# Kernel tuning notes

Hardware: AMD Instinct MI355X
Metric: run time of the kernel (lower is better)

Reference implementation:

```python
import jax, jax.numpy as jnp
import numpy as np

# static config (mirrors init_kwargs)
FS = 512          # frame_seqlen
NFPB = 2          # num_frame_per_block
NIB = 3           # num image/action/state blocks
NAPB = 32         # num_action_per_block
NSPB = 1          # num_state_per_block
LOCAL = 4         # local_attn_size (frames)
FIRST = FS
IMGB = NIB * NFPB * FS
ALEN = NIB * NAPB
SLEN = NIB * NSPB
TOTAL = FIRST + IMGB + ALEN + SLEN   # 3683
DIM = 1536
NH = 12
HD = DIM // NH    # 128
EPS = 1e-6


def _build_mask():
    # faithful port of _visualize_attention_mask (the block-sparse pattern)
    m = np.zeros((TOTAL, TOTAL), dtype=bool)
    fi0, fi1 = 0, FIRST
    ib0, ib1 = fi1, fi1 + IMGB
    a0, a1 = ib1, ib1 + ALEN
    s0 = a1
    m[fi0:fi1, fi0:fi1] = True  # first image: self only (sink)
    for b in range(NIB):
        bs = ib0 + b * NFPB * FS
        be = ib0 + (b + 1) * NFPB * FS
        m[bs:be, fi0:fi1] = True                      # sink
        kv = max(ib0, be - LOCAL * FS)                # local window
        m[bs:be, kv:be] = True
        m[bs:be, a0 + b * NAPB:a0 + (b + 1) * NAPB] = True
        m[bs:be, s0 + b * NSPB:s0 + (b + 1) * NSPB] = True
    for b in range(NIB):
        ab0 = a0 + b * NAPB
        ab1 = a0 + (b + 1) * NAPB
        m[ab0:ab1, fi0:fi1] = True
        ibe = ib0 + (b + 1) * NFPB * FS
        kv = max(ib0, ibe - LOCAL * FS)
        m[ab0:ab1, kv:ibe] = True
        m[ab0:ab1, ab0:ab1] = True
        m[ab0:ab1, s0 + b * NSPB:s0 + (b + 1) * NSPB] = True
    for b in range(NIB):
        ss = s0 + b * NSPB
        se = s0 + (b + 1) * NSPB
        m[ss:se, ss:se] = True
    return m

_MASK = jnp.asarray(_build_mask())


def _rms_norm(x, g):
    # WanRMSNorm over full dim, fp32 accumulation
    v = jnp.mean(jnp.square(x.astype(jnp.float32)), axis=-1, keepdims=True)
    return (x.astype(jnp.float32) * jax.lax.rsqrt(v + EPS)).astype(x.dtype) * g


def _rope(x, cos, sin):
    # x: [B,L,n,hd]; pairs are consecutive (..., hd//2, 2)
    B, L, n, d = x.shape
    xp = x.reshape(B, L, n, d // 2, 2)
    xr, xi = xp[..., 0], xp[..., 1]
    c = cos[None, :, None, :]
    s = sin[None, :, None, :]
    yr = xr * c - xi * s
    yi = xr * s + xi * c
    return jnp.stack([yr, yi], axis=-1).reshape(B, L, n, d)


def setup_inputs() -> dict:
    key = jax.random.key(0)
    ks = jax.random.split(key, 16)
    x = jax.random.normal(ks[0], (1, TOTAL, DIM), jnp.float32)

    def mkfreq(k, L):
        ang = jax.random.uniform(k, (L, HD // 2), jnp.float32, 0.0, 2.0 * np.pi)
        return jnp.stack([jnp.cos(ang), jnp.sin(ang)], axis=-1).reshape(L, HD)

    freqs = mkfreq(ks[1], FIRST + IMGB)
    freqs_action = mkfreq(ks[2], ALEN)
    freqs_state = mkfreq(ks[3], SLEN)
    sc = 1.0 / np.sqrt(DIM)
    Wq = jax.random.normal(ks[4], (DIM, DIM), jnp.float32) * sc
    Wk = jax.random.normal(ks[5], (DIM, DIM), jnp.float32) * sc
    Wv = jax.random.normal(ks[6], (DIM, DIM), jnp.float32) * sc
    Wo = jax.random.normal(ks[7], (DIM, DIM), jnp.float32) * sc
    bq = jax.random.normal(ks[8], (DIM,), jnp.float32) * 0.01
    bk = jax.random.normal(ks[9], (DIM,), jnp.float32) * 0.01
    bv = jax.random.normal(ks[10], (DIM,), jnp.float32) * 0.01
    bo = jax.random.normal(ks[11], (DIM,), jnp.float32) * 0.01
    gq = jnp.ones((DIM,), jnp.float32)
    gk = jnp.ones((DIM,), jnp.float32)
    return {"x": x, "freqs": freqs, "freqs_action": freqs_action,
            "freqs_state": freqs_state, "Wq": Wq, "bq": bq, "Wk": Wk, "bk": bk,
            "Wv": Wv, "bv": bv, "Wo": Wo, "bo": bo, "gq": gq, "gk": gk}


def reference(x, freqs, freqs_action, freqs_state, Wq, bq, Wk, bk, Wv, bv, Wo, bo, gq, gk):
    B, L, _ = x.shape
    q = _rms_norm(x @ Wq + bq, gq).reshape(B, L, NH, HD)
    k = _rms_norm(x @ Wk + bk, gk).reshape(B, L, NH, HD)
    v = (x @ Wv + bv).reshape(B, L, NH, HD)
    # full-sequence rope: image freqs then action freqs then state freqs
    f = jnp.concatenate([freqs, freqs_action, freqs_state], axis=0).reshape(L, HD // 2, 2)
    cos, sin = f[..., 0], f[..., 1]
    q = _rope(q, cos, sin)
    k = _rope(k, cos, sin)
    scores = jnp.einsum('bqnd,bknd->bnqk', q, k) / np.sqrt(HD)
    scores = jnp.where(_MASK[None, None], scores, jnp.finfo(scores.dtype).min)
    p = jax.nn.softmax(scores, axis=-1)
    o = jnp.einsum('bnqk,bknd->bqnd', p, v).reshape(B, L, DIM)
    return o @ Wo + bo
```

## Files before the change

kernel.cpp:

```cpp
#include <hip/hip_runtime.h>

#define LSEQ 3683
#define LPAD 3840
#define DIMSZ 1536
#define NHEAD 12
#define HEADD 128
#define SM_SCALE 0.088388347648318447f

typedef unsigned short u16;
typedef unsigned int u32;
typedef __bf16 bf16x8 __attribute__((ext_vector_type(8)));
typedef float f32x4 __attribute__((ext_vector_type(4)));

__device__ __forceinline__ u16 f2b(float f) {
  u32 u = __float_as_uint(f);
  u += 0x7FFFu + ((u >> 16) & 1u);
  return (u16)(u >> 16);
}
__device__ __forceinline__ float b2f(u16 s) {
  return __uint_as_float(((u32)s) << 16);
}
__device__ __forceinline__ int imax(int a, int b) { return a > b ? a : b; }

__device__ __forceinline__ void gl_lds16(const u16* g, u16* l) {
  __builtin_amdgcn_global_load_lds((const __attribute__((address_space(1))) u32*)g,
                                   (__attribute__((address_space(3))) u32*)l,
                                   16, 0, 0);
}

__device__ __forceinline__ int xcd_swz(int orig, int nwg) {
  int q = nwg >> 3, r = nwg & 7;
  int x = orig & 7, l = orig >> 3;
  return (x < r ? x * (q + 1) : r * (q + 1) + (x - r) * q) + l;
}

__global__ void convert_x_kernel(const float* __restrict__ x, u16* __restrict__ xb) {
  long idx = (long)blockIdx.x * blockDim.x + threadIdx.x;
  long base = idx * 4;
  if (base >= (long)LPAD * DIMSZ) return;
  float4 v;
  if (base < (long)LSEQ * DIMSZ) v = *(const float4*)(x + base);
  else v = make_float4(0.f, 0.f, 0.f, 0.f);
  ushort4 o;
  o.x = f2b(v.x); o.y = f2b(v.y); o.z = f2b(v.z); o.w = f2b(v.w);
  *(ushort4*)(xb + base) = o;
}

__global__ void transpose_w_kernel(const float* __restrict__ W0, const float* __restrict__ W1,
                                   const float* __restrict__ W2, const float* __restrict__ W3,
                                   u16* __restrict__ Wt) {
  const float* W = (blockIdx.z == 0) ? W0 : (blockIdx.z == 1) ? W1 : (blockIdx.z == 2) ? W2 : W3;
  u16* dst = Wt + (size_t)blockIdx.z * DIMSZ * DIMSZ;
  __shared__ float tile[32][33];
  int k0 = blockIdx.x * 32, n0 = blockIdx.y * 32;
  int tx = threadIdx.x & 31, ty = threadIdx.x >> 5;
  #pragma unroll
  for (int i = 0; i < 4; i++) {
    int k = k0 + ty + i * 8;
    tile[ty + i * 8][tx] = W[(size_t)k * DIMSZ + n0 + tx];
  }
  __syncthreads();
  #pragma unroll
  for (int i = 0; i < 4; i++) {
    int n = n0 + ty + i * 8;
    dst[(size_t)n * DIMSZ + k0 + tx] = f2b(tile[tx][ty + i * 8]);
  }
}

#define BAR() __builtin_amdgcn_s_barrier()
#define LGK0() asm volatile("s_waitcnt lgkmcnt(0)" ::: "memory")
#define LGK8() asm volatile("s_waitcnt lgkmcnt(8)" ::: "memory")
#define VMC9() asm volatile("s_waitcnt vmcnt(9)" ::: "memory")
#define VMC6() asm volatile("s_waitcnt vmcnt(6)" ::: "memory")
#define VMC0() asm volatile("s_waitcnt vmcnt(0)" ::: "memory")
#define PRIO1() __builtin_amdgcn_s_setprio(1)
#define PRIO0() __builtin_amdgcn_s_setprio(0)

#define STG_A(buf, q, kt) \
  gl_lds16(gA + (size_t)((q) * 64) * DIMSZ + (kt), &Asg[buf][((q) * 64 + w * 8) * 64]);
#define STG_B(buf, q, kt) \
  gl_lds16(gB + (size_t)((q) * 64) * DIMSZ + (kt), &Bsg[buf][((q) * 64 + w * 8) * 64]);

#define LDA3(buf, mh) { \
  _Pragma("unroll") for (int mf = 0; mf < 3; mf++) { \
    int rb = (wm * 96 + (mh) * 48 + mf * 16) * 64; \
    Ar[mf * 2 + 0] = *(const bf16x8*)&Asg[buf][rb + off0]; \
    Ar[mf * 2 + 1] = *(const bf16x8*)&Asg[buf][rb + off1]; } }
#define LDB3(buf, nh) { \
  _Pragma("unroll") for (int nf = 0; nf < 3; nf++) { \
    int rb = (wn * 96 + (nh) * 48 + nf * 16) * 64; \
    Br[nh][nf * 2 + 0] = *(const bf16x8*)&Bsg[buf][rb + off0]; \
    Br[nh][nf * 2 + 1] = *(const bf16x8*)&Bsg[buf][rb + off1]; } }

#define MFMAQ3(mh, nh) { \
  _Pragma("unroll") for (int mf = 0; mf < 3; mf++) \
    _Pragma("unroll") for (int nf = 0; nf < 3; nf++) { \
      acc[(mh)*3+mf][(nh)*3+nf] = __builtin_amdgcn_mfma_f32_16x16x32_bf16(Ar[mf*2+0], Br[nh][nf*2+0], acc[(mh)*3+mf][(nh)*3+nf], 0, 0, 0); \
      acc[(mh)*3+mf][(nh)*3+nf] = __builtin_amdgcn_mfma_f32_16x16x32_bf16(Ar[mf*2+1], Br[nh][nf*2+1], acc[(mh)*3+mf][(nh)*3+nf], 0, 0, 0); } }

__launch_bounds__(512, 2)
__global__ void gemm_qkv384_kernel(const u16* __restrict__ A, const u16* __restrict__ Wt,
                                   const float* __restrict__ bq, const float* __restrict__ bk,
                                   const float* __restrict__ bv,
                                   u16* __restrict__ Qb, u16* __restrict__ Kb,
                                   u16* __restrict__ Vt) {
  __shared__ __align__(16) u16 Asg[2][384 * 64];
  __shared__ __align__(16) u16 Bsg[2][192 * 64];

  int wg = xcd_swz(blockIdx.x, 10 * 24);
  int nt = wg % 24;
  int m0 = (wg / 24) * 384;
  int which = nt >> 3;
  const float* bias = (which == 0) ? bq : (which == 1) ? bk : bv;

  int t = threadIdx.x;
  int lane = t & 63, w = t >> 6;
  int c = lane & 15, g = lane >> 4;
  int wm = w >> 1, wn = w & 1;

  int srow = t >> 3;
  int schunk = ((t & 7) ^ (srow & 7)) * 8;
  const u16* gA = A + (size_t)(m0 + srow) * DIMSZ + schunk;
  const u16* gB = Wt + (size_t)(nt * 192 + srow) * DIMSZ + schunk;

  int off0 = c * 64 + ((g) ^ (c & 7)) * 8;
  int off1 = c * 64 + ((g + 4) ^ (c & 7)) * 8;

  f32x4 acc[6][6];
  f32x4 zero = {0.f, 0.f, 0.f, 0.f};
  #pragma unroll
  for (int am = 0; am < 6; am++)
    #pragma unroll
    for (int an = 0; an < 6; an++) acc[am][an] = zero;
  bf16x8 Ar[6];
  bf16x8 Br[2][6];

  STG_B(0, 0, 0) STG_B(0, 1, 0) STG_B(0, 2, 0)
  STG_A(0, 0, 0) STG_A(0, 1, 0) STG_A(0, 2, 0)
  STG_A(0, 3, 0) STG_A(0, 4, 0) STG_A(0, 5, 0)
  STG_B(1, 0, 64) STG_B(1, 1, 64) STG_B(1, 2, 64)
  STG_A(1, 0, 64) STG_A(1, 1, 64) STG_A(1, 2, 64)
  STG_A(1, 3, 64) STG_A(1, 4, 64) STG_A(1, 5, 64)
  VMC9();
  BAR();

  for (int i = 0; i < DIMSZ / 64 / 2 - 1; ++i) {
    int kt2 = (2 * i + 2) * 64;
    int kt3 = (2 * i + 3) * 64;
    LDA3(0, 0) LDB3(0, 0)
    LGK8(); BAR(); LGK0();
    PRIO1(); MFMAQ3(0, 0) PRIO0();
    BAR();
    LDB3(0, 1)
    BAR(); LGK0();
    PRIO1(); MFMAQ3(0, 1) PRIO0();
    BAR();
    LDA3(0, 1)
    STG_B(0, 0, kt2) STG_B(0, 1, kt2) STG_B(0, 2, kt2)
    BAR(); LGK0();
    PRIO1(); MFMAQ3(1, 1) PRIO0();
    BAR();
    STG_A(0, 0, kt2) STG_A(0, 1, kt2) STG_A(0, 2, kt2)
    VMC6(); BAR();
    PRIO1(); MFMAQ3(1, 0) PRIO0();
    BAR();
    LDA3(1, 0) LDB3(1, 0)
    STG_A(0, 3, kt2) STG_A(0, 4, kt2) STG_A(0, 5, kt2)
    LGK8(); BAR(); LGK0();
    PRIO1(); MFMAQ3(0, 0) PRIO0();
    BAR();
    LDB3(1, 1)
    BAR(); LGK0();
    PRIO1(); MFMAQ3(0, 1) PRIO0();
    BAR();
    LDA3(1, 1)
    STG_B(1, 0, kt3) STG_B(1, 1, kt3) STG_B(1, 2, kt3)
    BAR(); LGK0();
    PRIO1(); MFMAQ3(1, 1) PRIO0();
    BAR();
    STG_A(1, 0, kt3) STG_A(1, 1, kt3) STG_A(1, 2, kt3)
    STG_A(1, 3, kt3) STG_A(1, 4, kt3) STG_A(1, 5, kt3)
    VMC9(); BAR();
    PRIO1(); MFMAQ3(1, 0) PRIO0();
    BAR();
  }

  {
    LDA3(0, 0) LDB3(0, 0)
    LGK8(); BAR(); LGK0();
    PRIO1(); MFMAQ3(0, 0) PRIO0();
    BAR();
    LDB3(0, 1)
    BAR(); LGK0();
    PRIO1(); MFMAQ3(0, 1) PRIO0();
    BAR();
    LDA3(0, 1)
    BAR(); LGK0();
    PRIO1(); MFMAQ3(1, 1) PRIO0();
    BAR();
    VMC0(); BAR();
    PRIO1(); MFMAQ3(1, 0) PRIO0();
    BAR();
    LDA3(1, 0) LDB3(1, 0)
    LGK8(); BAR(); LGK0();
    PRIO1(); MFMAQ3(0, 0) PRIO0();
    BAR();
    LDB3(1, 1)
    BAR(); LGK0();
    PRIO1(); MFMAQ3(0, 1) PRIO0();
    BAR();
    LDA3(1, 1)
    BAR(); LGK0();
    PRIO1(); MFMAQ3(1, 1) PRIO0();
    MFMAQ3(1, 0)
  }

  #pragma unroll
  for (int an = 0; an < 6; an++) {
    int ncol = (nt & 7) * 192 + wn * 96 + (an / 3) * 48 + (an % 3) * 16 + c;
    float bvv = bias[ncol];
    #pragma unroll
    for (int am = 0; am < 6; am++) {
      int rowb = m0 + wm * 96 + (am / 3) * 48 + (am % 3) * 16 + 4 * g;
      if (which == 2) {
        ushort4 pv;
        pv.x = f2b(acc[am][an][0] + bvv);
        pv.y = f2b(acc[am][an][1] + bvv);
        pv.z = f2b(acc[am][an][2] + bvv);
        pv.w = f2b(acc[am][an][3] + bvv);
        *(ushort4*)&Vt[(size_t)ncol * LPAD + rowb] = pv;
      } else {
        u16* P = (which == 1) ? Kb : Qb;
        #pragma unroll
        for (int r = 0; r < 4; r++)
          P[(size_t)(rowb + r) * DIMSZ + ncol] = f2b(acc[am][an][r] + bvv);
      }
    }
  }
}

#define GEMM_PROLOGUE()                                                          \
  __shared__ __align__(16) u16 As[4][128 * 32];                                  \
  __shared__ __align__(16) u16 Bs[4][128 * 32];                                  \
  int t = threadIdx.x;                                                           \
  int lane = t & 63, w = t >> 6;                                                 \
  int g = lane >> 4, c = lane & 15;                                              \
  int wm = w >> 1, wn = w & 1;                                                   \
  f32x4 acc[4][4];                                                               \
  f32x4 zero = {0.f, 0.f, 0.f, 0.f};                                             \
  _Pragma("unroll") for (int fr = 0; fr < 4; fr++)                               \
      _Pragma("unroll") for (int fc = 0; fc < 4; fc++) acc[fr][fc] = zero;       \
  int srcc = (((lane & 3) ^ ((lane >> 2) & 3))) * 8;    \
  const u16* gA = A + (size_t)(m0 + w * 32 + (lane >> 2)) * DIMSZ + srcc;        \
  const u16* gB = Bt + (size_t)(n0 + w * 32 + (lane >> 2)) * DIMSZ + srcc;       \
  int gsw = (g ^ (c & 3)) * 8;

#define GEMM_STAGE(buf, kt)                                                      \
  _Pragma("unroll") for (int q = 0; q < 2; q++) {                                \
    gl_lds16(gA + (size_t)(q * 16) * DIMSZ + (kt), &As[buf][(w * 32 + q * 16) * 32]); \
    gl_lds16(gB + (size_t)(q * 16) * DIMSZ + (kt), &Bs[buf][(w * 32 + q * 16) * 32]); \
  }

#define GEMM_COMPUTE(buf)                                                        \
  {                                                                              \
    bf16x8 af[4], bfr[4];                                                        \
    _Pragma("unroll") for (int fr = 0; fr < 4; fr++)                             \
        af[fr] = *(const bf16x8*)&As[buf][(wm * 64 + fr * 16 + c) * 32 + gsw];   \
    _Pragma("unroll") for (int fc = 0; fc < 4; fc++)                             \
        bfr[fc] = *(const bf16x8*)&Bs[buf][(wn * 64 + fc * 16 + c) * 32 + gsw];  \
    _Pragma("unroll") for (int fr = 0; fr < 4; fr++)                             \
        _Pragma("unroll") for (int fc = 0; fc < 4; fc++)                         \
            acc[fr][fc] = __builtin_amdgcn_mfma_f32_16x16x32_bf16(af[fr], bfr[fc], acc[fr][fc], 0, 0, 0); \
  }

#define GEMM_MAINLOOP()                                                          \
  GEMM_STAGE(0, 0)                                                               \
  GEMM_STAGE(1, 32)                                                              \
  GEMM_STAGE(2, 64)                                                              \
  {                                                                              \
    const int nk = DIMSZ / 32;                                                   \
    for (int ki = 0; ki < nk; ki++) {                                            \
      int rem = nk - ki;                                                         \
      if (rem > 2)      asm volatile("s_waitcnt vmcnt(8)" ::: "memory");         \
      else if (rem == 2) asm volatile("s_waitcnt vmcnt(4)" ::: "memory");        \
      else               asm volatile("s_waitcnt vmcnt(0)" ::: "memory");        \
      __builtin_amdgcn_s_barrier();                                              \
      if (ki + 3 < nk) { GEMM_STAGE((ki + 3) & 3, (ki + 3) * 32) }               \
      GEMM_COMPUTE(ki & 3)                                                       \
    }                                                                            \
  }

__launch_bounds__(256)
__global__ void gemm_out_kernel(const u16* __restrict__ A, const u16* __restrict__ Bt,
                                const float* __restrict__ bias, float* __restrict__ outF) {
  int wg = xcd_swz(blockIdx.x, 29 * 12);
  int n0 = (wg % 12) * 128;
  int m0 = (wg / 12) * 128;

  GEMM_PROLOGUE()
  GEMM_MAINLOOP()

  #pragma unroll
  for (int fc = 0; fc < 4; fc++) {
    int col = n0 + wn * 64 + fc * 16 + c;
    float bvv = bias[col];
    #pragma unroll
    for (int fr = 0; fr < 4; fr++) {
      int rowb = m0 + wm * 64 + fr * 16 + 4 * g;
      #pragma unroll
      for (int r = 0; r < 4; r++) {
        int row = rowb + r;
        if (row < LSEQ) outF[(size_t)row * DIMSZ + col] = acc[fr][fc][r] + bvv;
      }
    }
  }
}

__launch_bounds__(256)
__global__ void normrope_kernel(u16* __restrict__ Qb, u16* __restrict__ Kb,
                                const float* __restrict__ gq, const float* __restrict__ gk,
                                const float* __restrict__ freqs, const float* __restrict__ freqs_a,
                                const float* __restrict__ freqs_s) {
  int l = blockIdx.x;
  int sel = blockIdx.y;
  u16* P = sel ? Kb : Qb;
  const float* gvec = sel ? gk : gq;
  int t = threadIdx.x;
  u16* row = P + (size_t)l * DIMSZ;
  float xv[6];
  #pragma unroll
  for (int i = 0; i < 3; i++) {
    int p = i * 256 + t;
    ushort2 u = *(const ushort2*)(row + 2 * p);
    xv[2 * i] = b2f(u.x);
    xv[2 * i + 1] = b2f(u.y);
  }
  float ss = 0.f;
  #pragma unroll
  for (int i = 0; i < 6; i++) ss += xv[i] * xv[i];
  #pragma unroll
  for (int d = 32; d; d >>= 1) ss += __shfl_down(ss, d);
  __shared__ float red[4];
  __shared__ float rshare;
  if ((t & 63) == 0) red[t >> 6] = ss;
  __syncthreads();
  if (t == 0) rshare = rsqrtf((red[0] + red[1] + red[2] + red[3]) * (1.0f / DIMSZ) + 1e-6f);
  __syncthreads();
  float rms = rshare;

  const float* f = (l < 3584) ? (freqs + (size_t)l * HEADD)
                : (l < 3680) ? (freqs_a + (size_t)(l - 3584) * HEADD)
                             : (freqs_s + (size_t)(l - 3680) * HEADD);
  #pragma unroll
  for (int i = 0; i < 3; i++) {
    int p = i * 256 + t;
    int j = p & 63;
    float2 csn = *(const float2*)(f + 2 * j);
    float2 gv = *(const float2*)(gvec + 2 * p);
    float xr = xv[2 * i] * rms * gv.x;
    float xi = xv[2 * i + 1] * rms * gv.y;
    ushort2 o;
    o.x = f2b(xr * csn.x - xi * csn.y);
    o.y = f2b(xr * csn.y + xi * csn.x);
    *(ushort2*)(row + 2 * p) = o;
  }
}

#define PSLOT_U16 16640
__launch_bounds__(256, 2)
__global__ void attn_dense_kernel(const u16* __restrict__ Q, const u16* __restrict__ K,
                                  const u16* __restrict__ Vt, u16* __restrict__ O,
                                  u16* __restrict__ DP) {
  __shared__ __align__(16) u16 Ks[2][32 * 144];
  __shared__ __align__(16) u16 Vs[2][128 * 40];
  __shared__ __align__(16) u16 Pl[4][32 * 40];

  int bx = blockIdx.x;
  int qbase, h, part, nparts, fb;
  if (bx < 48) { qbase = (bx / 12) * 128; h = bx % 12; part = 0; nparts = 1; fb = -1; }
  else if (bx < 336) { int i = bx - 48; int qb = i / 36; h = (i / 3) % 12; part = i % 3; nparts = 3; fb = 0; qbase = 512 + qb * 128; }
  else if (bx < 720) { int i = bx - 336; int qb = i / 48; h = (i / 4) % 12; part = i % 4; nparts = 4; fb = 1; qbase = 1536 + qb * 128; }
  else { int i = bx - 720; int qb = i / 48; h = (i / 4) % 12; part = i % 4; nparts = 4; fb = 2; qbase = 2560 + qb * 128; }

  int S0, E0, S1, E1, S2, E2, S3, E3, niv;
  if (fb < 0) { S0 = 0; E0 = 512; S1 = E1 = S2 = E2 = S3 = E3 = 0; niv = 1; }
  else {
    int be = 512 + (fb + 1) * 1024;
    int kv = imax(512, be - 2048);
    S0 = 0; E0 = 512; S1 = kv; E1 = be;
    S2 = 3584 + 32 * fb; E2 = S2 + 32; S3 = 3680 + fb; E3 = S3 + 1; niv = 4;
  }
  int B0 = S0 & ~31, B1 = S1 & ~31, B2 = S2 & ~31, B3 = S3 & ~31;
  int T1 = (E0 - B0 + 31) >> 5;
  int T2 = T1 + ((niv > 1) ? ((E1 - B1 + 31) >> 5) : 0);
  int T3 = T2 + ((niv > 2) ? ((E2 - B2 + 31) >> 5) : 0);
  int T4 = T3 + ((niv > 3) ? ((E3 - B3 + 31) >> 5) : 0);
  int ntile = T4;
  int rlo = (ntile * part) / nparts, rhi = (ntile * (part + 1)) / nparts;

  auto tile_of = [&](int f, int& k0, int& lo, int& hi) {
    k0 = B0 + (f << 5); lo = S0; hi = E0;
    if (niv > 1 && f >= T1) { k0 = B1 + ((f - T1) << 5); lo = S1; hi = E1; }
    if (niv > 2 && f >= T2) { k0 = B2 + ((f - T2) << 5); lo = S2; hi = E2; }
    if (niv > 3 && f >= T3) { k0 = B3 + ((f - T3) << 5); lo = S3; hi = E3; }
  };

  int T = threadIdx.x;
  int lane = T & 63, w = T >> 6, g = lane >> 4, c = lane & 15;

  const u16* kgp = K + (size_t)(T >> 3) * DIMSZ + h * HEADD + 8 * (T & 7);
  int kds = (T >> 3) * 144 + 8 * (T & 7);
  const u16* vgp = Vt + ((size_t)h * HEADD + (T >> 1)) * LPAD + 16 * (T & 1);
  int vds = (T >> 1) * 40 + 16 * (T & 1);

  uint4 sk0, sk1, sv0, sv1;
  auto stage_load = [&](int k0) {
    const u16* kp = kgp + (size_t)k0 * DIMSZ;
    sk0 = *(const uint4*)(kp);
    sk1 = *(const uint4*)(kp + 64);
    sv0 = *(const uint4*)(vgp + k0);
    sv1 = *(const uint4*)(vgp + k0 + 8);
  };
  auto stage_write = [&](int buf) {
    *(uint4*)&Ks[buf][kds] = sk0;
    *(uint4*)&Ks[buf][kds + 64] = sk1;
    *(uint4*)&Vs[buf][vds] = sv0;
    *(uint4*)&Vs[buf][vds + 8] = sv1;
  };

  int qrow0 = qbase + 32 * w;
  bf16x8 qf[2][4];
  #pragma unroll
  for (int a = 0; a < 2; a++) {
    const u16* qp = Q + (size_t)(qrow0 + a * 16 + c) * DIMSZ + h * HEADD + 8 * g;
    #pragma unroll
    for (int s = 0; s < 4; s++) qf[a][s] = *(const bf16x8*)(qp + 32 * s);
  }

  f32x4 zero = {0.f, 0.f, 0.f, 0.f};
  f32x4 acc[2][8];
  f32x4 lacc[2];
  #pragma unroll
  for (int a = 0; a < 2; a++) {
    lacc[a] = zero;
    #pragma unroll
    for (int cc = 0; cc < 8; cc++) acc[a][cc] = zero;
  }
  bf16x8 onesv;
  {
    u16 ob = 0x3F80;
    #pragma unroll
    for (int i = 0; i < 8; i++) onesv[i] = ((const __bf16*)&ob)[0];
  }

  u16* Pw = &Pl[w][0];
  const float c1 = SM_SCALE * 1.44269504088896340f;
  const float c2 = 12.0f * 1.44269504088896340f;

  {
    int k0, lo, hi; tile_of(rlo, k0, lo, hi);
    stage_load(k0);
    stage_write(0);
  }
  __syncthreads();
  int cur = 0;

  for (int t = rlo; t < rhi; ++t) {
    int ck0, clo, chi; tile_of(t, ck0, clo, chi);
    bool pre = (t + 1 < rhi);
    if (pre) { int nk0, nl, nh; tile_of(t + 1, nk0, nl, nh); stage_load(nk0); }

    f32x4 sc[2][2];
    sc[0][0] = zero; sc[0][1] = zero; sc[1][0] = zero; sc[1][1] = zero;
    #pragma unroll
    for (int k2 = 0; k2 < 2; k2++)
      #pragma unroll
      for (int s = 0; s < 4; s++) {
        bf16x8 kf = *(const bf16x8*)&Ks[cur][(16 * k2 + c) * 144 + 32 * s + 8 * g];
        sc[0][k2] = __builtin_amdgcn_mfma_f32_16x16x32_bf16(qf[0][s], kf, sc[0][k2], 0, 0, 0);
        sc[1][k2] = __builtin_amdgcn_mfma_f32_16x16x32_bf16(qf[1][s], kf, sc[1][k2], 0, 0, 0);
      }

    #pragma unroll
    for (int a = 0; a < 2; a++)
      #pragma unroll
      for (int k2 = 0; k2 < 2; k2++) {
        int k = ck0 + k2 * 16 + c;
        bool valid = (k >= clo) && (k < chi);
        #pragma unroll
        for (int r = 0; r < 4; r++) {
          float p = exp2f(sc[a][k2][r] * c1 - c2);
          Pw[(a * 16 + 4 * g + r) * 40 + k2 * 16 + c] = valid ? f2b(p) : (u16)0;
        }
      }
    asm volatile("s_waitcnt lgkmcnt(0)" ::: "memory");
    __builtin_amdgcn_sched_barrier(0);

    bf16x8 pa0 = *(const bf16x8*)&Pw[c * 40 + 8 * g];
    bf16x8 pa1 = *(const bf16x8*)&Pw[(16 + c) * 40 + 8 * g];

    #pragma unroll
    for (int cc = 0; cc < 8; cc++) {
      bf16x8 vf = *(const bf16x8*)&Vs[cur][(cc * 16 + c) * 40 + 8 * g];
      acc[0][cc] = __builtin_amdgcn_mfma_f32_16x16x32_bf16(pa0, vf, acc[0][cc], 0, 0, 0);
      acc[1][cc] = __builtin_amdgcn_mfma_f32_16x16x32_bf16(pa1, vf, acc[1][cc], 0, 0, 0);
    }
    lacc[0] = __builtin_amdgcn_mfma_f32_16x16x32_bf16(pa0, onesv, lacc[0], 0, 0, 0);
    lacc[1] = __builtin_amdgcn_mfma_f32_16x16x32_bf16(pa1, onesv, lacc[1], 0, 0, 0);

    if (pre) stage_write(cur ^ 1);
    __syncthreads();
    cur ^= 1;
  }

  if (nparts == 1) {
    float inv[2][4];
    #pragma unroll
    for (int a = 0; a < 2; a++)
      #pragma unroll
      for (int r = 0; r < 4; r++) inv[a][r] = (lacc[a][r] > 0.f) ? 1.0f / lacc[a][r] : 0.f;
    #pragma unroll
    for (int a = 0; a < 2; a++)
      #pragma unroll
      for (int cc = 0; cc < 8; cc++)
        #pragma unroll
        for (int r = 0; r < 4; r++) {
          int row = qrow0 + a * 16 + 4 * g + r;
          O[(size_t)row * DIMSZ + h * HEADD + cc * 16 + c] = f2b(acc[a][cc][r] * inv[a][r]);
        }
  } else {
    int qb = (qbase - 512 - fb * 1024) >> 7;
    int sbase = (fb == 0) ? 0 : (fb == 1 ? 288 : 672);
    int slot = sbase + (qb * 12 + h) * nparts + part;
    u16* DPs = DP + (size_t)slot * PSLOT_U16;
    float* lout = (float*)(DPs + 16384);
    #pragma unroll
    for (int a = 0; a < 2; a++) {
      #pragma unroll
      for (int cc = 0; cc < 8; cc++)
        #pragma unroll
        for (int r = 0; r < 4; r++)
          DPs[(32 * w + a * 16 + 4 * g + r) * 128 + cc * 16 + c] = f2b(acc[a][cc][r]);
      if (c == 0)
        #pragma unroll
        for (int r = 0; r < 4; r++) lout[32 * w + a * 16 + 4 * g + r] = lacc[a][r];
    }
  }
}

__launch_bounds__(256)
__global__ void attn_merge_dense(const u16* __restrict__ DP, u16* __restrict__ O) {
  int qi = blockIdx.x, h = blockIdx.y;
  int fb = qi >> 3, qb = qi & 7;
  int nparts = (fb == 0) ? 3 : 4;
  int sbase = (fb == 0) ? 0 : (fb == 1 ? 288 : 672);
  int slot0 = sbase + (qb * 12 + h) * nparts;
  int qbase = 512 + fb * 1024 + qb * 128;
  int T = threadIdx.x;
  int row = T >> 1, c0 = 64 * (T & 1);

  float sum[64];
  #pragma unroll
  for (int j = 0; j < 64; j++) sum[j] = 0.f;
  float l = 0.f;
  for (int p = 0; p < nparts; p++) {
    const u16* S = DP + (size_t)(slot0 + p) * PSLOT_U16;
    l += ((const float*)(S + 16384))[row];
    #pragma unroll
    for (int j = 0; j < 64; j += 8) {
      uint4 v = *(const uint4*)&S[row * 128 + c0 + j];
      const u16* pv = (const u16*)&v;
      #pragma unroll
      for (int q = 0; q < 8; q++) sum[j + q] += b2f(pv[q]);
    }
  }
  float inv = (l > 0.f) ? 1.0f / l : 0.f;
  u16 tmp[64];
  #pragma unroll
  for (int j = 0; j < 64; j++) tmp[j] = f2b(sum[j] * inv);
  u16* op = O + (size_t)(qbase + row) * DIMSZ + h * HEADD + c0;
  #pragma unroll
  for (int j = 0; j < 64; j += 8) *(uint4*)(op + j) = *(uint4*)&tmp[j];
}

__launch_bounds__(256, 2)
__global__ void attn_tail_kernel(const u16* __restrict__ Q, const u16* __restrict__ K,
                                 const u16* __restrict__ Vt, u16* __restrict__ O,
                                 float* __restrict__ Part) {
  __shared__ __align__(16) char smem[20608];
  __shared__ float Lsum[32];

  int bx = blockIdx.x;
  int h = blockIdx.y;
  int qt, part;
  if (bx < 3) { qt = 112 + bx; part = 0; }
  else if (bx < 6) { qt = 112 + (bx - 3); part = 1; }
  else { qt = 115; part = 0; }
  int qbase = qt * 32;
  bool heavy = (qt <= 114);

  int t = threadIdx.x, lane = t & 63, w = t >> 6, g = lane >> 4, c = lane & 15;

  int S0, E0, S1, E1, S2, E2, S3, E3, niv;
  if (qbase < 3680) {
    int b = (qbase - 3584) >> 5;
    int ibe = 512 + (b + 1) * 1024;
    int kv = imax(512, ibe - 2048);
    S0 = 0; E0 = 512; S1 = kv; E1 = ibe;
    S2 = 3584 + 32 * b; E2 = S2 + 32; S3 = 3680 + b; E3 = S3 + 1; niv = 4;
  } else {
    S0 = 3680; E0 = 3683; S1 = S2 = S3 = 0; E1 = E2 = E3 = 0; niv = 1;
  }
  bool diag = (qbase >= 3680);

  int B0 = S0 & ~31, B1 = S1 & ~31, B2 = S2 & ~31, B3 = S3 & ~31;
  int T1 = (E0 - B0 + 31) >> 5;
  int T2 = T1 + ((niv > 1) ? ((E1 - B1 + 31) >> 5) : 0);
  int T3 = T2 + ((niv > 2) ? ((E2 - B2 + 31) >> 5) : 0);
  int T4 = T3 + ((niv > 3) ? ((E3 - B3 + 31) >> 5) : 0);
  int ntile = T4;

  int rlo = 0, rhi = ntile;
  if (heavy) { int half = (ntile + 1) >> 1; if (part == 0) rhi = half; else rlo = half; }

  auto tile_of = [&](int f, int& k0, int& lo, int& hi) {
    k0 = B0 + (f << 5); lo = S0; hi = E0;
    if (niv > 1 && f >= T1) { k0 = B1 + ((f - T1) << 5); lo = S1; hi = E1; }
    if (niv > 2 && f >= T2) { k0 = B2 + ((f - T2) << 5); lo = S2; hi = E2; }
    if (niv > 3 && f >= T3) { k0 = B3 + ((f - T3) << 5); lo = S3; hi = E3; }
  };

  bf16x8 qf[2][4];
  #pragma unroll
  for (int a = 0; a < 2; a++) {
    const u16* qp = Q + (size_t)(qbase + a * 16 + c) * DIMSZ + h * HEADD + 8 * g;
    #pragma unroll
    for (int s = 0; s < 4; s++) qf[a][s] = *(const bf16x8*)(qp + 32 * s);
  }

  f32x4 zero = {0.f, 0.f, 0.f, 0.f};
  f32x4 acc[2][8];
  f32x4 lacc[2];
  #pragma unroll
  for (int a = 0; a < 2; a++) {
    lacc[a] = zero;
    #pragma unroll
    for (int cc = 0; cc < 8; cc++) acc[a][cc] = zero;
  }
  bf16x8 onesv;
  {
    u16 ob = 0x3F80;
    #pragma unroll
    for (int i = 0; i < 8; i++) onesv[i] = ((const __bf16*)&ob)[0];
  }

  u16* PwA = (u16*)smem + w * 2560;
  u16* PwB = PwA + 1280;

  bf16x8 kc[2][4], vbuf[8], pa0, pa1;
  const float c1 = SM_SCALE * 1.44269504088896340f;
  const float c2 = 12.0f * 1.44269504088896340f;

  auto loadK = [&](int k0) {
    #pragma unroll
    for (int k2 = 0; k2 < 2; k2++) {
      const u16* kp = K + (size_t)(k0 + 16 * k2 + c) * DIMSZ + h * HEADD + 8 * g;
      #pragma unroll
      for (int s = 0; s < 4; s++) kc[k2][s] = *(const bf16x8*)(kp + 32 * s);
    }
  };
  auto loadV = [&](int k0) {
    #pragma unroll
    for (int cc = 0; cc < 8; cc++)
      vbuf[cc] = *(const bf16x8*)(Vt + (size_t)(h * HEADD + cc * 16 + c) * LPAD + k0 + 8 * g);
  };
  auto QKf = [&](f32x4 (&sc)[2][2]) {
    sc[0][0] = zero; sc[0][1] = zero; sc[1][0] = zero; sc[1][1] = zero;
    #pragma unroll
    for (int k2 = 0; k2 < 2; k2++)
      #pragma unroll
      for (int s = 0; s < 4; s++) {
        sc[0][k2] = __builtin_amdgcn_mfma_f32_16x16x32_bf16(qf[0][s], kc[k2][s], sc[0][k2], 0, 0, 0);
        sc[1][k2] = __builtin_amdgcn_mfma_f32_16x16x32_bf16(qf[1][s], kc[k2][s], sc[1][k2], 0, 0, 0);
      }
  };
  auto smstore = [&](f32x4 (&sc)[2][2], int k0, int lo, int hi, u16* Pw) {
    #pragma unroll
    for (int a = 0; a < 2; a++)
      #pragma unroll
      for (int k2 = 0; k2 < 2; k2++) {
        int k = k0 + k2 * 16 + c;
        bool valid = (k >= lo) && (k < hi);
        #pragma unroll
        for (int r = 0; r < 4; r++) {
          float p = exp2f(sc[a][k2][r] * c1 - c2);
          bool v = valid;
          if (diag) { int qr = qbase + a * 16 + 4 * g + r; v = v && (k == qr); }
          Pw[(a * 16 + 4 * g + r) * 40 + k2 * 16 + c] = v ? f2b(p) : (u16)0;
        }
      }
  };
  auto readP = [&](u16* Pw) {
    pa0 = *(const bf16x8*)&Pw[c * 40 + 8 * g];
    pa1 = *(const bf16x8*)&Pw[(16 + c) * 40 + 8 * g];
  };
  auto PV = [&]() {
    #pragma unroll
    for (int cc = 0; cc < 8; cc++) {
      acc[0][cc] = __builtin_amdgcn_mfma_f32_16x16x32_bf16(pa0, vbuf[cc], acc[0][cc], 0, 0, 0);
      acc[1][cc] = __builtin_amdgcn_mfma_f32_16x16x32_bf16(pa1, vbuf[cc], acc[1][cc], 0, 0, 0);
    }
    lacc[0] = __builtin_amdgcn_mfma_f32_16x16x32_bf16(pa0, onesv, lacc[0], 0, 0, 0);
    lacc[1] = __builtin_amdgcn_mfma_f32_16x16x32_bf16(pa1, onesv, lacc[1], 0, 0, 0);
  };

  int i = rlo + w;
  if (i < rhi) {
    int ik0, ilo, ihi; tile_of(i, ik0, ilo, ihi);
    loadK(ik0);
    loadV(ik0);
    {
      f32x4 sc[2][2]; QKf(sc);
      smstore(sc, ik0, ilo, ihi, PwA);
    }
    asm volatile("s_waitcnt lgkmcnt(0)" ::: "memory");
    __builtin_amdgcn_sched_barrier(0);
    readP(PwA);
    int nx = i + 4;
    int nk0 = 0, nlo = 0, nhi = 0;
    bool useB = true;
    if (nx < rhi) { tile_of(nx, nk0, nlo, nhi); loadK(nk0); }
    while (nx < rhi) {
      int ck0 = nk0, clo = nlo, chi = nhi;
      f32x4 sc[2][2]; QKf(sc);
      int nn = nx + 4;
      if (nn < rhi) { tile_of(nn, nk0, nlo, nhi); loadK(nk0); }
      u16* Pw = useB ? PwB : PwA;
      smstore(sc, ck0, clo, chi, Pw);
      PV();
      loadV(ck0);
      asm volatile("s_waitcnt lgkmcnt(0)" ::: "memory");
      __builtin_amdgcn_sched_barrier(0);
      readP(Pw);
      useB = !useB;
      i = nx; nx = nn;
    }
    PV();
  }

  __syncthreads();
  float* Oacc = (float*)smem;
  if (w == 0) {
    #pragma unroll
    for (int a = 0; a < 2; a++) {
      #pragma unroll
      for (int cc = 0; cc < 8; cc++)
        #pragma unroll
        for (int r = 0; r < 4; r++)
          Oacc[(a * 16 + 4 * g + r) * 132 + cc * 16 + c] = acc[a][cc][r];
      if (c == 0)
        #pragma unroll
        for (int r = 0; r < 4; r++) Lsum[a * 16 + 4 * g + r] = lacc[a][r];
    }
  }
  __syncthreads();
  #pragma unroll
  for (int ww = 1; ww < 4; ww++) {
    if (w == ww) {
      #pragma unroll
      for (int a = 0; a < 2; a++) {
        #pragma unroll
        for (int cc = 0; cc < 8; cc++)
          #pragma unroll
          for (int r = 0; r < 4; r++)
            Oacc[(a * 16 + 4 * g + r) * 132 + cc * 16 + c] += acc[a][cc][r];
        if (c == 0)
          #pragma unroll
          for (int r = 0; r < 4; r++) Lsum[a * 16 + 4 * g + r] += lacc[a][r];
      }
    }
    __syncthreads();
  }

  int row = t >> 3, c0 = (t & 7) * 16;
  if (heavy) {
    size_t slot = ((size_t)((qt - 112) * 12 + h)) * 2 + part;
    float* P = Part + slot * 4160;
    #pragma unroll
    for (int j = 0; j < 16; j += 4)
      *(float4*)&P[row * 128 + c0 + j] = *(float4*)&Oacc[row * 132 + c0 + j];
    if ((t & 7) == 0) P[4096 + row] = Lsum[row];
  } else {
    int orow = qbase + row;
    if (orow < LSEQ) {
      float lsv = Lsum[row];
      float inv = (lsv > 0.f) ? 1.0f / lsv : 0.f;
      u16 tmp[16];
      #pragma unroll
      for (int j = 0; j < 16; j++) tmp[j] = f2b(Oacc[row * 132 + c0 + j] * inv);
      u16* op = O + (size_t)orow * DIMSZ + h * HEADD + c0;
      *(uint4*)(op) = *(uint4*)&tmp[0];
      *(uint4*)(op + 8) = *(uint4*)&tmp[8];
    }
  }
}

__launch_bounds__(256)
__global__ void attn_merge_tail(const float* __restrict__ Part, u16* __restrict__ O) {
  int b = blockIdx.x, h = blockIdx.y;
  const float* A = Part + ((size_t)(b * 12 + h)) * 2 * 4160;
  const float* B = A + 4160;
  int t = threadIdx.x;
  int row = t >> 3, c0 = (t & 7) * 16;
  float l = A[4096 + row] + B[4096 + row];
  float inv = (l > 0.f) ? 1.0f / l : 0.f;
  int orow = 3584 + b * 32 + row;
  u16 tmp[16];
  #pragma unroll
  for (int jj = 0; jj < 16; jj += 4) {
    float4 va = *(const float4*)&A[row * 128 + c0 + jj];
    float4 vb = *(const float4*)&B[row * 128 + c0 + jj];
    tmp[jj + 0] = f2b((va.x + vb.x) * inv);
    tmp[jj + 1] = f2b((va.y + vb.y) * inv);
    tmp[jj + 2] = f2b((va.z + vb.z) * inv);
    tmp[jj + 3] = f2b((va.w + vb.w) * inv);
  }
  u16* op = O + (size_t)orow * DIMSZ + h * HEADD + c0;
  *(uint4*)(op) = *(uint4*)&tmp[0];
  *(uint4*)(op + 8) = *(uint4*)&tmp[8];
}

extern "C" void kernel_launch(void* const* d_in, const int* in_sizes, int n_in,
                              void* d_out, int out_size, void* d_ws, size_t ws_size,
                              hipStream_t stream) {
  (void)in_sizes; (void)n_in; (void)out_size; (void)ws_size;
  const float* x       = (const float*)d_in[0];
  const float* freqs   = (const float*)d_in[1];
  const float* freqs_a = (const float*)d_in[2];
  const float* freqs_s = (const float*)d_in[3];
  const float* Wq = (const float*)d_in[4];
  const float* bq = (const float*)d_in[5];
  const float* Wk = (const float*)d_in[6];
  const float* bk = (const float*)d_in[7];
  const float* Wv = (const float*)d_in[8];
  const float* bv = (const float*)d_in[9];
  const float* Wo = (const float*)d_in[10];
  const float* bo = (const float*)d_in[11];
  const float* gq = (const float*)d_in[12];
  const float* gk = (const float*)d_in[13];
  float* out = (float*)d_out;

  char* ws = (char*)d_ws;
  size_t off = 0;
  auto alloc = [&](size_t bytes) -> void* {
    void* p = ws + off;
    off += (bytes + 255) & ~(size_t)255;
    return p;
  };
  u16* xb   = (u16*)alloc((size_t)LPAD * DIMSZ * 2);
  u16* Wt   = (u16*)alloc((size_t)4 * DIMSZ * DIMSZ * 2);
  u16* Qb   = (u16*)alloc((size_t)LPAD * DIMSZ * 2);
  u16* Kb   = (u16*)alloc((size_t)LPAD * DIMSZ * 2);
  u16* Vt   = (u16*)alloc((size_t)DIMSZ * LPAD * 2);
  u16* Ob   = (u16*)alloc((size_t)LPAD * DIMSZ * 2);
  u16* DP   = (u16*)alloc((size_t)1056 * PSLOT_U16 * 2);
  float* PartT = (float*)alloc((size_t)3 * 12 * 2 * 4160 * 4);

  convert_x_kernel<<<(LPAD * DIMSZ / 4 + 255) / 256, 256, 0, stream>>>(x, xb);
  transpose_w_kernel<<<dim3(48, 48, 4), 256, 0, stream>>>(Wq, Wk, Wv, Wo, Wt);

  gemm_qkv384_kernel<<<dim3(240), 512, 0, stream>>>(xb, Wt, bq, bk, bv, Qb, Kb, Vt);

  normrope_kernel<<<dim3(LSEQ, 2), 256, 0, stream>>>(Qb, Kb, gq, gk, freqs, freqs_a, freqs_s);

  attn_dense_kernel<<<dim3(1104), 256, 0, stream>>>(Qb, Kb, Vt, Ob, DP);
  attn_tail_kernel<<<dim3(7, 12), 256, 0, stream>>>(Qb, Kb, Vt, Ob, PartT);
  attn_merge_dense<<<dim3(24, 12), 256, 0, stream>>>(DP, Ob);
  attn_merge_tail<<<dim3(3, 12), 256, 0, stream>>>(PartT, Ob);

  gemm_out_kernel<<<dim3(29 * 12), 256, 0, stream>>>(Ob, Wt + 3 * (size_t)DIMSZ * DIMSZ, bo, out);
}
```

Before: 256.6 us.

## Reuse 384x192 pipelined GEMM for output projection and streamline softmax exp

The QKV GEMM body is factored into a macro and reused for the output projection, which now runs 80 large 384x192 tiles with 512 threads instead of 348 128x128 tiles. The attention kernels switch to the hardware exp2 intrinsic, add a fast path that skips per-element masking when a key chunk is fully valid, and shrink the K shared-memory row pitch from 144 to 136. The output GEMM trades block count for per-block reuse, so the GPU may be underfilled with only 80 workgroups. The changed K pitch alters the LDS bank-conflict pattern, and the exp2 intrinsic gives slightly different precision.

```diff
diff --git a/kernel.cpp b/kernel.cpp
--- a/kernel.cpp
+++ b/kernel.cpp
@@ -98,6 +98,85 @@
       acc[(mh)*3+mf][(nh)*3+nf] = __builtin_amdgcn_mfma_f32_16x16x32_bf16(Ar[mf*2+0], Br[nh][nf*2+0], acc[(mh)*3+mf][(nh)*3+nf], 0, 0, 0); \
       acc[(mh)*3+mf][(nh)*3+nf] = __builtin_amdgcn_mfma_f32_16x16x32_bf16(Ar[mf*2+1], Br[nh][nf*2+1], acc[(mh)*3+mf][(nh)*3+nf], 0, 0, 0); } }
 
+#define GEMM384_BODY() \
+  STG_B(0, 0, 0) STG_B(0, 1, 0) STG_B(0, 2, 0) \
+  STG_A(0, 0, 0) STG_A(0, 1, 0) STG_A(0, 2, 0) \
+  STG_A(0, 3, 0) STG_A(0, 4, 0) STG_A(0, 5, 0) \
+  STG_B(1, 0, 64) STG_B(1, 1, 64) STG_B(1, 2, 64) \
+  STG_A(1, 0, 64) STG_A(1, 1, 64) STG_A(1, 2, 64) \
+  STG_A(1, 3, 64) STG_A(1, 4, 64) STG_A(1, 5, 64) \
+  VMC9(); \
+  BAR(); \
+  for (int i = 0; i < DIMSZ / 64 / 2 - 1; ++i) { \
+    int kt2 = (2 * i + 2) * 64; \
+    int kt3 = (2 * i + 3) * 64; \
+    LDA3(0, 0) LDB3(0, 0) \
+    LGK8(); BAR(); LGK0(); \
+    PRIO1(); MFMAQ3(0, 0) PRIO0(); \
+    BAR(); \
+    LDB3(0, 1) \
+    BAR(); LGK0(); \
+    PRIO1(); MFMAQ3(0, 1) PRIO0(); \
+    BAR(); \
+    LDA3(0, 1) \
+    STG_B(0, 0, kt2) STG_B(0, 1, kt2) STG_B(0, 2, kt2) \
+    BAR(); LGK0(); \
+    PRIO1(); MFMAQ3(1, 1) PRIO0(); \
+    BAR(); \
+    STG_A(0, 0, kt2) STG_A(0, 1, kt2) STG_A(0, 2, kt2) \
+    VMC6(); BAR(); \
+    PRIO1(); MFMAQ3(1, 0) PRIO0(); \
+    BAR(); \
+    LDA3(1, 0) LDB3(1, 0) \
+    STG_A(0, 3, kt2) STG_A(0, 4, kt2) STG_A(0, 5, kt2) \
+    LGK8(); BAR(); LGK0(); \
+    PRIO1(); MFMAQ3(0, 0) PRIO0(); \
+    BAR(); \
+    LDB3(1, 1) \
+    BAR(); LGK0(); \
+    PRIO1(); MFMAQ3(0, 1) PRIO0(); \
+    BAR(); \
+    LDA3(1, 1) \
+    STG_B(1, 0, kt3) STG_B(1, 1, kt3) STG_B(1, 2, kt3) \
+    BAR(); LGK0(); \
+    PRIO1(); MFMAQ3(1, 1) PRIO0(); \
+    BAR(); \
+    STG_A(1, 0, kt3) STG_A(1, 1, kt3) STG_A(1, 2, kt3) \
+    STG_A(1, 3, kt3) STG_A(1, 4, kt3) STG_A(1, 5, kt3) \
+    VMC9(); BAR(); \
+    PRIO1(); MFMAQ3(1, 0) PRIO0(); \
+    BAR(); \
+  } \
+  { \
+    LDA3(0, 0) LDB3(0, 0) \
+    LGK8(); BAR(); LGK0(); \
+    PRIO1(); MFMAQ3(0, 0) PRIO0(); \
+    BAR(); \
+    LDB3(0, 1) \
+    BAR(); LGK0(); \
+    PRIO1(); MFMAQ3(0, 1) PRIO0(); \
+    BAR(); \
+    LDA3(0, 1) \
+    BAR(); LGK0(); \
+    PRIO1(); MFMAQ3(1, 1) PRIO0(); \
+    BAR(); \
+    VMC0(); BAR(); \
+    PRIO1(); MFMAQ3(1, 0) PRIO0(); \
+    BAR(); \
+    LDA3(1, 0) LDB3(1, 0) \
+    LGK8(); BAR(); LGK0(); \
+    PRIO1(); MFMAQ3(0, 0) PRIO0(); \
+    BAR(); \
+    LDB3(1, 1) \
+    BAR(); LGK0(); \
+    PRIO1(); MFMAQ3(0, 1) PRIO0(); \
+    BAR(); \
+    LDA3(1, 1) \
+    BAR(); LGK0(); \
+    PRIO1(); MFMAQ3(1, 1) PRIO0(); \
+    MFMAQ3(1, 0) \
+  }
+
 __launch_bounds__(512, 2)
 __global__ void gemm_qkv384_kernel(const u16* __restrict__ A, const u16* __restrict__ Wt,
                                    const float* __restrict__ bq, const float* __restrict__ bk,
@@ -135,85 +214,7 @@
   bf16x8 Ar[6];
   bf16x8 Br[2][6];
 
-  STG_B(0, 0, 0) STG_B(0, 1, 0) STG_B(0, 2, 0)
-  STG_A(0, 0, 0) STG_A(0, 1, 0) STG_A(0, 2, 0)
-  STG_A(0, 3, 0) STG_A(0, 4, 0) STG_A(0, 5, 0)
-  STG_B(1, 0, 64) STG_B(1, 1, 64) STG_B(1, 2, 64)
-  STG_A(1, 0, 64) STG_A(1, 1, 64) STG_A(1, 2, 64)
-  STG_A(1, 3, 64) STG_A(1, 4, 64) STG_A(1, 5, 64)
-  VMC9();
-  BAR();
-
-  for (int i = 0; i < DIMSZ / 64 / 2 - 1; ++i) {
-    int kt2 = (2 * i + 2) * 64;
-    int kt3 = (2 * i + 3) * 64;
-    LDA3(0, 0) LDB3(0, 0)
-    LGK8(); BAR(); LGK0();
-    PRIO1(); MFMAQ3(0, 0) PRIO0();
-    BAR();
-    LDB3(0, 1)
-    BAR(); LGK0();
-    PRIO1(); MFMAQ3(0, 1) PRIO0();
-    BAR();
-    LDA3(0, 1)
-    STG_B(0, 0, kt2) STG_B(0, 1, kt2) STG_B(0, 2, kt2)
-    BAR(); LGK0();
-    PRIO1(); MFMAQ3(1, 1) PRIO0();
-    BAR();
-    STG_A(0, 0, kt2) STG_A(0, 1, kt2) STG_A(0, 2, kt2)
-    VMC6(); BAR();
-    PRIO1(); MFMAQ3(1, 0) PRIO0();
-    BAR();
-    LDA3(1, 0) LDB3(1, 0)
-    STG_A(0, 3, kt2) STG_A(0, 4, kt2) STG_A(0, 5, kt2)
-    LGK8(); BAR(); LGK0();
-    PRIO1(); MFMAQ3(0, 0) PRIO0();
-    BAR();
-    LDB3(1, 1)
-    BAR(); LGK0();
-    PRIO1(); MFMAQ3(0, 1) PRIO0();
-    BAR();
-    LDA3(1, 1)
-    STG_B(1, 0, kt3) STG_B(1, 1, kt3) STG_B(1, 2, kt3)
-    BAR(); LGK0();
-    PRIO1(); MFMAQ3(1, 1) PRIO0();
-    BAR();
-    STG_A(1, 0, kt3) STG_A(1, 1, kt3) STG_A(1, 2, kt3)
-    STG_A(1, 3, kt3) STG_A(1, 4, kt3) STG_A(1, 5, kt3)
-    VMC9(); BAR();
-    PRIO1(); MFMAQ3(1, 0) PRIO0();
-    BAR();
-  }
-
-  {
-    LDA3(0, 0) LDB3(0, 0)
-    LGK8(); BAR(); LGK0();
-    PRIO1(); MFMAQ3(0, 0) PRIO0();
-    BAR();
-    LDB3(0, 1)
-    BAR(); LGK0();
-    PRIO1(); MFMAQ3(0, 1) PRIO0();
-    BAR();
-    LDA3(0, 1)
-    BAR(); LGK0();
-    PRIO1(); MFMAQ3(1, 1) PRIO0();
-    BAR();
-    VMC0(); BAR();
-    PRIO1(); MFMAQ3(1, 0) PRIO0();
-    BAR();
-    LDA3(1, 0) LDB3(1, 0)
-    LGK8(); BAR(); LGK0();
-    PRIO1(); MFMAQ3(0, 0) PRIO0();
-    BAR();
-    LDB3(1, 1)
-    BAR(); LGK0();
-    PRIO1(); MFMAQ3(0, 1) PRIO0();
-    BAR();
-    LDA3(1, 1)
-    BAR(); LGK0();
-    PRIO1(); MFMAQ3(1, 1) PRIO0();
-    MFMAQ3(1, 0)
-  }
+  GEMM384_BODY()
 
   #pragma unroll
   for (int an = 0; an < 6; an++) {
@@ -239,78 +240,51 @@
   }
 }
 
-#define GEMM_PROLOGUE()                                                          \
-  __shared__ __align__(16) u16 As[4][128 * 32];                                  \
-  __shared__ __align__(16) u16 Bs[4][128 * 32];                                  \
-  int t = threadIdx.x;                                                           \
-  int lane = t & 63, w = t >> 6;                                                 \
-  int g = lane >> 4, c = lane & 15;                                              \
-  int wm = w >> 1, wn = w & 1;                                                   \
-  f32x4 acc[4][4];                                                               \
-  f32x4 zero = {0.f, 0.f, 0.f, 0.f};                                             \
-  _Pragma("unroll") for (int fr = 0; fr < 4; fr++)                               \
-      _Pragma("unroll") for (int fc = 0; fc < 4; fc++) acc[fr][fc] = zero;       \
-  int srcc = (((lane & 3) ^ ((lane >> 2) & 3))) * 8;    \
-  const u16* gA = A + (size_t)(m0 + w * 32 + (lane >> 2)) * DIMSZ + srcc;        \
-  const u16* gB = Bt + (size_t)(n0 + w * 32 + (lane >> 2)) * DIMSZ + srcc;       \
-  int gsw = (g ^ (c & 3)) * 8;
-
-#define GEMM_STAGE(buf, kt)                                                      \
-  _Pragma("unroll") for (int q = 0; q < 2; q++) {                                \
-    gl_lds16(gA + (size_t)(q * 16) * DIMSZ + (kt), &As[buf][(w * 32 + q * 16) * 32]); \
-    gl_lds16(gB + (size_t)(q * 16) * DIMSZ + (kt), &Bs[buf][(w * 32 + q * 16) * 32]); \
-  }
-
-#define GEMM_COMPUTE(buf)                                                        \
-  {                                                                              \
-    bf16x8 af[4], bfr[4];                                                        \
-    _Pragma("unroll") for (int fr = 0; fr < 4; fr++)                             \
-        af[fr] = *(const bf16x8*)&As[buf][(wm * 64 + fr * 16 + c) * 32 + gsw];   \
-    _Pragma("unroll") for (int fc = 0; fc < 4; fc++)                             \
-        bfr[fc] = *(const bf16x8*)&Bs[buf][(wn * 64 + fc * 16 + c) * 32 + gsw];  \
-    _Pragma("unroll") for (int fr = 0; fr < 4; fr++)                             \
-        _Pragma("unroll") for (int fc = 0; fc < 4; fc++)                         \
-            acc[fr][fc] = __builtin_amdgcn_mfma_f32_16x16x32_bf16(af[fr], bfr[fc], acc[fr][fc], 0, 0, 0); \
-  }
-
-#define GEMM_MAINLOOP()                                                          \
-  GEMM_STAGE(0, 0)                                                               \
-  GEMM_STAGE(1, 32)                                                              \
-  GEMM_STAGE(2, 64)                                                              \
-  {                                                                              \
-    const int nk = DIMSZ / 32;                                                   \
-    for (int ki = 0; ki < nk; ki++) {                                            \
-      int rem = nk - ki;                                                         \
-      if (rem > 2)      asm volatile("s_waitcnt vmcnt(8)" ::: "memory");         \
-      else if (rem == 2) asm volatile("s_waitcnt vmcnt(4)" ::: "memory");        \
-      else               asm volatile("s_waitcnt vmcnt(0)" ::: "memory");        \
-      __builtin_amdgcn_s_barrier();                                              \
-      if (ki + 3 < nk) { GEMM_STAGE((ki + 3) & 3, (ki + 3) * 32) }               \
-      GEMM_COMPUTE(ki & 3)                                                       \
-    }                                                                            \
-  }
-
-__launch_bounds__(256)
-__global__ void gemm_out_kernel(const u16* __restrict__ A, const u16* __restrict__ Bt,
-                                const float* __restrict__ bias, float* __restrict__ outF) {
-  int wg = xcd_swz(blockIdx.x, 29 * 12);
-  int n0 = (wg % 12) * 128;
-  int m0 = (wg / 12) * 128;
-
-  GEMM_PROLOGUE()
-  GEMM_MAINLOOP()
-
-  #pragma unroll
-  for (int fc = 0; fc < 4; fc++) {
-    int col = n0 + wn * 64 + fc * 16 + c;
-    float bvv = bias[col];
-    #pragma unroll
-    for (int fr = 0; fr < 4; fr++) {
-      int rowb = m0 + wm * 64 + fr * 16 + 4 * g;
+__launch_bounds__(512, 2)
+__global__ void gemm_out384_kernel(const u16* __restrict__ A, const u16* __restrict__ Bt,
+                                   const float* __restrict__ bias, float* __restrict__ outF) {
+  __shared__ __align__(16) u16 Asg[2][384 * 64];
+  __shared__ __align__(16) u16 Bsg[2][192 * 64];
+
+  int wg = xcd_swz(blockIdx.x, 10 * 8);
+  int nt = wg % 8;
+  int m0 = (wg / 8) * 384;
+
+  int t = threadIdx.x;
+  int lane = t & 63, w = t >> 6;
+  int c = lane & 15, g = lane >> 4;
+  int wm = w >> 1, wn = w & 1;
+
+  int srow = t >> 3;
+  int schunk = ((t & 7) ^ (srow & 7)) * 8;
+  const u16* gA = A + (size_t)(m0 + srow) * DIMSZ + schunk;
+  const u16* gB = Bt + (size_t)(nt * 192 + srow) * DIMSZ + schunk;
+
+  int off0 = c * 64 + ((g) ^ (c & 7)) * 8;
+  int off1 = c * 64 + ((g + 4) ^ (c & 7)) * 8;
+
+  f32x4 acc[6][6];
+  f32x4 zero = {0.f, 0.f, 0.f, 0.f};
+  #pragma unroll
+  for (int am = 0; am < 6; am++)
+    #pragma unroll
+    for (int an = 0; an < 6; an++) acc[am][an] = zero;
+  bf16x8 Ar[6];
+  bf16x8 Br[2][6];
+
+  GEMM384_BODY()
+
+  #pragma unroll
+  for (int an = 0; an < 6; an++) {
+    int ncol = nt * 192 + wn * 96 + (an / 3) * 48 + (an % 3) * 16 + c;
+    float bvv = bias[ncol];
+    #pragma unroll
+    for (int am = 0; am < 6; am++) {
+      int rowb = m0 + wm * 96 + (am / 3) * 48 + (am % 3) * 16 + 4 * g;
       #pragma unroll
       for (int r = 0; r < 4; r++) {
         int row = rowb + r;
-        if (row < LSEQ) outF[(size_t)row * DIMSZ + col] = acc[fr][fc][r] + bvv;
+        if (row < LSEQ) outF[(size_t)row * DIMSZ + ncol] = acc[am][an][r] + bvv;
       }
     }
   }
@@ -371,7 +345,7 @@
 __global__ void attn_dense_kernel(const u16* __restrict__ Q, const u16* __restrict__ K,
                                   const u16* __restrict__ Vt, u16* __restrict__ O,
                                   u16* __restrict__ DP) {
-  __shared__ __align__(16) u16 Ks[2][32 * 144];
+  __shared__ __align__(16) u16 Ks[2][32 * 136];
   __shared__ __align__(16) u16 Vs[2][128 * 40];
   __shared__ __align__(16) u16 Pl[4][32 * 40];
 
@@ -409,7 +383,7 @@
   int lane = T & 63, w = T >> 6, g = lane >> 4, c = lane & 15;
 
   const u16* kgp = K + (size_t)(T >> 3) * DIMSZ + h * HEADD + 8 * (T & 7);
-  int kds = (T >> 3) * 144 + 8 * (T & 7);
+  int kds = (T >> 3) * 136 + 8 * (T & 7);
   const u16* vgp = Vt + ((size_t)h * HEADD + (T >> 1)) * LPAD + 16 * (T & 1);
   int vds = (T >> 1) * 40 + 16 * (T & 1);
 
@@ -476,23 +450,35 @@
     for (int k2 = 0; k2 < 2; k2++)
       #pragma unroll
       for (int s = 0; s < 4; s++) {
-        bf16x8 kf = *(const bf16x8*)&Ks[cur][(16 * k2 + c) * 144 + 32 * s + 8 * g];
+        bf16x8 kf = *(const bf16x8*)&Ks[cur][(16 * k2 + c) * 136 + 32 * s + 8 * g];
         sc[0][k2] = __builtin_amdgcn_mfma_f32_16x16x32_bf16(qf[0][s], kf, sc[0][k2], 0, 0, 0);
         sc[1][k2] = __builtin_amdgcn_mfma_f32_16x16x32_bf16(qf[1][s], kf, sc[1][k2], 0, 0, 0);
       }
 
-    #pragma unroll
-    for (int a = 0; a < 2; a++)
-      #pragma unroll
-      for (int k2 = 0; k2 < 2; k2++) {
-        int k = ck0 + k2 * 16 + c;
-        bool valid = (k >= clo) && (k < chi);
-        #pragma unroll
-        for (int r = 0; r < 4; r++) {
-          float p = exp2f(sc[a][k2][r] * c1 - c2);
-          Pw[(a * 16 + 4 * g + r) * 40 + k2 * 16 + c] = valid ? f2b(p) : (u16)0;
+    if (ck0 >= clo && ck0 + 32 <= chi) {
+      #pragma unroll
+      for (int a = 0; a < 2; a++)
+        #pragma unroll
+        for (int k2 = 0; k2 < 2; k2++)
+          #pragma unroll
+          for (int r = 0; r < 4; r++) {
+            float p = __builtin_amdgcn_exp2f(sc[a][k2][r] * c1 - c2);
+            Pw[(a * 16 + 4 * g + r) * 40 + k2 * 16 + c] = f2b(p);
+          }
+    } else {
+      #pragma unroll
+      for (int a = 0; a < 2; a++)
+        #pragma unroll
+        for (int k2 = 0; k2 < 2; k2++) {
+          int k = ck0 + k2 * 16 + c;
+          bool valid = (k >= clo) && (k < chi);
+          #pragma unroll
+          for (int r = 0; r < 4; r++) {
+            float p = __builtin_amdgcn_exp2f(sc[a][k2][r] * c1 - c2);
+            Pw[(a * 16 + 4 * g + r) * 40 + k2 * 16 + c] = valid ? f2b(p) : (u16)0;
+          }
         }
-      }
+    }
     asm volatile("s_waitcnt lgkmcnt(0)" ::: "memory");
     __builtin_amdgcn_sched_barrier(0);
 
@@ -693,7 +679,7 @@
         bool valid = (k >= lo) && (k < hi);
         #pragma unroll
         for (int r = 0; r < 4; r++) {
-          float p = exp2f(sc[a][k2][r] * c1 - c2);
+          float p = __builtin_amdgcn_exp2f(sc[a][k2][r] * c1 - c2);
           bool v = valid;
           if (diag) { int qr = qbase + a * 16 + 4 * g + r; v = v && (k == qr); }
           Pw[(a * 16 + 4 * g + r) * 40 + k2 * 16 + c] = v ? f2b(p) : (u16)0;
@@ -878,5 +864,5 @@
   attn_merge_dense<<<dim3(24, 12), 256, 0, stream>>>(DP, Ob);
   attn_merge_tail<<<dim3(3, 12), 256, 0, stream>>>(PartT, Ob);
 
-  gemm_out_kernel<<<dim3(29 * 12), 256, 0, stream>>>(Ob, Wt + 3 * (size_t)DIMSZ * DIMSZ, bo, out);
-}
+  gemm_out384_kernel<<<dim3(80), 512, 0, stream>>>(Ob, Wt + 3 * (size_t)DIMSZ * DIMSZ, bo, out);
+}
```

Measured after the change: 252.9 us. No clear change (-1.4%).
